# Performance work log

Hardware: AMD Instinct MI355X
Metric: run time of the kernel (lower is better)

## Reference

```python
import jax, jax.numpy as jnp
import numpy as np

RADIUS = 0.1
NSAMPLE = 32
NORMALIZE_XYZ = False
USE_XYZ = True


def ball_query(xyz, center_xyz, radius, nsample):
    """xyz: (B,N,3), center_xyz: (B,S,3) -> idx (B,S,nsample) int32.
    For each center, first `nsample` point indices within `radius`;
    slots with no valid point are filled with the first valid index (0 if none)."""
    N = xyz.shape[1]
    # squared distances (B,S,N)
    d2 = jnp.sum((center_xyz[:, :, None, :] - xyz[:, None, :, :]) ** 2, axis=-1)
    in_ball = d2 < radius * radius
    cand = jnp.where(in_ball, jnp.arange(N, dtype=jnp.int32)[None, None, :], jnp.int32(N))
    cand = jnp.sort(cand, axis=-1)[..., :nsample]  # first nsample in-ball indices
    first = cand[..., :1]
    first = jnp.where(first == N, 0, first)  # fallback to 0 if ball is empty
    idx = jnp.where(cand == N, first, cand)
    return idx


def group(features, idx):
    """features: (B,C,N), idx: (B,S,K) -> (B,C,S,K)"""
    return jax.vmap(lambda f, i: f[:, i])(features, idx)


def setup_inputs() -> dict:
    key = jax.random.key(0)
    k1, k2, k3 = jax.random.split(key, 3)
    B, N, S, C = 4, 8192, 2048, 64
    xyz = jax.random.uniform(k1, (B, N, 3), dtype=jnp.float32)
    center_xyz = jax.random.uniform(k2, (B, S, 3), dtype=jnp.float32)
    features = jax.random.normal(k3, (B, C, N), dtype=jnp.float32)
    return {"xyz": xyz, "center_xyz": center_xyz, "features": features}


def reference(xyz, center_xyz, features):
    idx = ball_query(xyz, center_xyz, RADIUS, NSAMPLE)  # (B,S,K)
    xyz_t = jnp.transpose(xyz, (0, 2, 1))  # (B,3,N)
    grouped_xyz = group(xyz_t, idx)  # (B,3,S,K)
    grouped_xyz = grouped_xyz - jnp.transpose(center_xyz, (0, 2, 1))[..., None]
    if NORMALIZE_XYZ:
        grouped_xyz = grouped_xyz / RADIUS
    grouped_features = group(features, idx)  # (B,C,S,K)
    if USE_XYZ:
        return jnp.concatenate([grouped_xyz, grouped_features], axis=1)  # (B,3+C,S,K)
    return grouped_features
```

## Files before the change

kernel.cpp:

```cpp
#include <hip/hip_runtime.h>
#include <stdint.h>

constexpr int N_PTS = 8192;
constexpr int S_CTR = 2048;
constexpr int BATCH = 4;
constexpr int CHANS = 64;
constexpr int KS = 32;
constexpr int CH_OUT = CHANS + 3;
constexpr int GD = 10;
constexpr int NCELL = GD * GD * GD;
constexpr int CAP = 128;

__device__ __forceinline__ int cell_of(float p) {
    int c = (int)((double)p * 10.0);
    return c < 0 ? 0 : (c > GD - 1 ? GD - 1 : c);
}

__global__ __launch_bounds__(1024) void grid_build(
    const float* __restrict__ xyz, int* __restrict__ cellStart,
    int* __restrict__ sIdx, float* __restrict__ sX,
    float* __restrict__ sY, float* __restrict__ sZ)
{
    __shared__ int cnts[NCELL];
    __shared__ int sc[1024];
    __shared__ int off[NCELL];
    const int b = blockIdx.x, t = threadIdx.x;
    const float* xb = xyz + (size_t)b * N_PTS * 3;

    for (int i = t; i < NCELL; i += 1024) cnts[i] = 0;
    __syncthreads();

    int cellr[8];
#pragma unroll
    for (int j = 0; j < 8; ++j) {
        const int i = t + j * 1024;
        const float x = xb[i * 3], y = xb[i * 3 + 1], z = xb[i * 3 + 2];
        const int c = (cell_of(z) * GD + cell_of(y)) * GD + cell_of(x);
        cellr[j] = c;
        atomicAdd(&cnts[c], 1);
    }
    __syncthreads();

    sc[t] = (t < NCELL) ? cnts[t] : 0;
    __syncthreads();
    for (int o = 1; o < 1024; o <<= 1) {
        const int v = (t >= o) ? sc[t - o] : 0;
        __syncthreads();
        sc[t] += v;
        __syncthreads();
    }
    const int excl = (t == 0) ? 0 : sc[t - 1];
    if (t < NCELL) { cellStart[b * (NCELL + 1) + t] = excl; off[t] = excl; }
    if (t == 0) cellStart[b * (NCELL + 1) + NCELL] = N_PTS;
    __syncthreads();

#pragma unroll
    for (int j = 0; j < 8; ++j) {
        const int i = t + j * 1024;
        const int pos = atomicAdd(&off[cellr[j]], 1);
        sIdx[b * N_PTS + pos] = i;
        sX[b * N_PTS + pos] = xb[i * 3];
        sY[b * N_PTS + pos] = xb[i * 3 + 1];
        sZ[b * N_PTS + pos] = xb[i * 3 + 2];
    }
}

__global__ __launch_bounds__(256) void bq_query(
    const float* __restrict__ ctr, const int* __restrict__ cellStart,
    const int* __restrict__ sIdx, const float* __restrict__ sX,
    const float* __restrict__ sY, const float* __restrict__ sZ,
    int* __restrict__ idx_out)
{
    __shared__ int cand[4][CAP];
    const int wave = threadIdx.x >> 6, lane = threadIdx.x & 63;
    const int cg = blockIdx.x * 4 + wave;
    const int b = cg >> 11;
    const float cx = ctr[(size_t)cg * 3];
    const float cy = ctr[(size_t)cg * 3 + 1];
    const float cz = ctr[(size_t)cg * 3 + 2];
    const float r2 = (float)(0.1 * 0.1);

    const int ix = cell_of(cx), iy = cell_of(cy), iz = cell_of(cz);
    const int xlo = max(ix - 1, 0), xhi = min(ix + 1, GD - 1);
    const int ylo = max(iy - 1, 0), yhi = min(iy + 1, GD - 1);
    const int zlo = max(iz - 1, 0), zhi = min(iz + 1, GD - 1);

    unsigned cnt = 0;
    const int csb = b * (NCELL + 1);
    const int pb = b * N_PTS;

    for (int zz = zlo; zz <= zhi; ++zz)
        for (int yy = ylo; yy <= yhi; ++yy) {
            const int rowc = (zz * GD + yy) * GD;
            const int rs = cellStart[csb + rowc + xlo];
            const int re = cellStart[csb + rowc + xhi + 1];
            for (int p0 = rs; p0 < re; p0 += 64) {
                const int i = p0 + lane;
                const bool valid = i < re;
                float px = 1e9f, py = 1e9f, pz = 1e9f; int oid = 0;
                if (valid) {
                    px = sX[pb + i]; py = sY[pb + i]; pz = sZ[pb + i];
                    oid = sIdx[pb + i];
                }
                const float dx = __fsub_rn(cx, px);
                const float dy = __fsub_rn(cy, py);
                const float dz = __fsub_rn(cz, pz);
                const float d2 = __fadd_rn(
                    __fadd_rn(__fmul_rn(dx, dx), __fmul_rn(dy, dy)),
                    __fmul_rn(dz, dz));
                const bool inb = valid && (d2 < r2);
                const unsigned long long mask = __ballot(inb);
                if (mask) {
                    const unsigned rank = __builtin_amdgcn_mbcnt_hi(
                        (unsigned)(mask >> 32),
                        __builtin_amdgcn_mbcnt_lo((unsigned)mask, 0u));
                    if (inb) {
                        const unsigned slot = cnt + rank;
                        if (slot < (unsigned)CAP) cand[wave][slot] = oid;
                    }
                    cnt += (unsigned)__popcll(mask);
                }
            }
        }
    if (cnt > (unsigned)CAP) cnt = CAP;

    int v0 = (lane < (int)cnt) ? cand[wave][lane] : 0x7fffffff;
    int v1 = (lane + 64 < (int)cnt) ? cand[wave][lane + 64] : 0x7fffffff;
#pragma unroll
    for (int k = 2; k <= 128; k <<= 1) {
        if (k == 128) {
            const int a = min(v0, v1); v1 = max(v0, v1); v0 = a;
        }
#pragma unroll
        for (int j = (k == 128 ? 32 : (k >> 1)); j >= 1; j >>= 1) {
            const int o0 = __shfl_xor(v0, j);
            const int o1 = __shfl_xor(v1, j);
            const bool lower = (lane & j) == 0;
            bool up0, up1;
            if (k == 64)       { up0 = true;  up1 = false; }
            else if (k == 128) { up0 = true;  up1 = true;  }
            else { const bool u = (lane & k) == 0; up0 = u; up1 = u; }
            v0 = (up0 == lower) ? min(v0, o0) : max(v0, o0);
            v1 = (up1 == lower) ? min(v1, o1) : max(v1, o1);
        }
    }

    int first = __shfl(v0, 0);
    if (cnt == 0u) first = 0;
    if (lane < KS) {
        const int val = (lane < (int)cnt) ? v0 : first;
        idx_out[(size_t)cg * KS + lane] = val;
    }
}

__global__ __launch_bounds__(256) void transpose_kernel(
    const float* __restrict__ feat, float* __restrict__ featT)
{
    __shared__ float tile[64][65];
    const int t = threadIdx.x;
    const int n0 = blockIdx.x * 64;
    const int b = blockIdx.y;
    const float* fb = feat + (size_t)b * CHANS * N_PTS;
#pragma unroll
    for (int r = 0; r < 16; ++r) {
        const int c = r * 4 + (t >> 6);
        tile[c][t & 63] = fb[(size_t)c * N_PTS + n0 + (t & 63)];
    }
    __syncthreads();
    float* ob = featT + ((size_t)b * N_PTS + n0) * CHANS;
#pragma unroll
    for (int r = 0; r < 16; ++r) {
        const int n = r * 4 + (t >> 6);
        ob[(size_t)n * CHANS + (t & 63)] = tile[t & 63][n];
    }
}

__global__ __launch_bounds__(256) void gather_kernel(
    const float* __restrict__ xyz, const float* __restrict__ ctr,
    const float* __restrict__ featT, const int* __restrict__ idx_ws,
    float* __restrict__ out)
{
    const int tg = blockIdx.x * 256 + threadIdx.x;
    const int cg = tg >> 5;
    const int k = tg & 31;
    const int b = cg >> 11;
    const int s = cg & (S_CTR - 1);
    const int id = idx_ws[(size_t)cg * KS + k];

    const float* pp = xyz + ((size_t)b * N_PTS + id) * 3;
    const float* cc = ctr + (size_t)cg * 3;
    const float g0 = __fsub_rn(pp[0], cc[0]);
    const float g1 = __fsub_rn(pp[1], cc[1]);
    const float g2 = __fsub_rn(pp[2], cc[2]);

    float f[CHANS];
    const float4* fr = (const float4*)(featT + ((size_t)b * N_PTS + id) * CHANS);
#pragma unroll
    for (int j = 0; j < CHANS / 4; ++j) {
        const float4 v = fr[j];
        f[j * 4 + 0] = v.x; f[j * 4 + 1] = v.y;
        f[j * 4 + 2] = v.z; f[j * 4 + 3] = v.w;
    }

    float* ob = out + ((size_t)b * CH_OUT * S_CTR + s) * KS + k;
    const size_t chs = (size_t)S_CTR * KS;
    ob[0] = g0;
    ob[chs] = g1;
    ob[2 * chs] = g2;
#pragma unroll
    for (int ch = 0; ch < CHANS; ++ch)
        ob[(size_t)(ch + 3) * chs] = f[ch];
}

__global__ __launch_bounds__(256) void bq_brute(
    const float* __restrict__ xyz, const float* __restrict__ ctr,
    int* __restrict__ idx_out)
{
    const int wave = threadIdx.x >> 6, lane = threadIdx.x & 63;
    const int cg = blockIdx.x * 4 + wave;
    const int b = cg >> 11;
    const float* xb = xyz + (size_t)b * N_PTS * 3;
    const float cx = ctr[(size_t)cg * 3], cy = ctr[(size_t)cg * 3 + 1],
                cz = ctr[(size_t)cg * 3 + 2];
    __shared__ int lidx[4][KS];
    unsigned cnt = 0;
    const float r2 = (float)(0.1 * 0.1);
    for (int n0 = 0; n0 < N_PTS && cnt < (unsigned)KS; n0 += 64) {
        const int n = n0 + lane;
        const float px = xb[n * 3], py = xb[n * 3 + 1], pz = xb[n * 3 + 2];
        const float dx = __fsub_rn(cx, px), dy = __fsub_rn(cy, py),
                    dz = __fsub_rn(cz, pz);
        const float d2 = __fadd_rn(
            __fadd_rn(__fmul_rn(dx, dx), __fmul_rn(dy, dy)), __fmul_rn(dz, dz));
        const bool inb = d2 < r2;
        const unsigned long long mask = __ballot(inb);
        if (mask) {
            const unsigned rank = __builtin_amdgcn_mbcnt_hi(
                (unsigned)(mask >> 32),
                __builtin_amdgcn_mbcnt_lo((unsigned)mask, 0u));
            const unsigned slot = cnt + rank;
            if (inb && slot < (unsigned)KS) lidx[wave][slot] = n;
            cnt += (unsigned)__popcll(mask);
        }
    }
    if (cnt > (unsigned)KS) cnt = KS;
    const int first = (cnt > 0) ? lidx[wave][0] : 0;
    if (lane < KS)
        idx_out[(size_t)cg * KS + lane] = (lane < (int)cnt) ? lidx[wave][lane] : first;
}

__global__ __launch_bounds__(256) void gather_direct(
    const float* __restrict__ xyz, const float* __restrict__ ctr,
    const float* __restrict__ feat, const int* __restrict__ idx_ws,
    float* __restrict__ out)
{
    const int wave = threadIdx.x >> 6, lane = threadIdx.x & 63;
    const int cg = blockIdx.x * 4 + wave;
    const int b = cg >> 11;
    const int s = cg & (S_CTR - 1);
    const int k = lane & 31;
    const int half = lane >> 5;
    const int id = idx_ws[(size_t)cg * KS + k];
    const float* pp = xyz + ((size_t)b * N_PTS + id) * 3;
    const float* cc = ctr + (size_t)cg * 3;
    const float g0 = __fsub_rn(pp[0], cc[0]);
    const float g1 = __fsub_rn(pp[1], cc[1]);
    const float g2 = __fsub_rn(pp[2], cc[2]);
    const float* fb = feat + (size_t)b * CHANS * N_PTS + id;
    float* ob = out + ((size_t)b * CH_OUT * S_CTR + s) * KS + k;
    const size_t chs = (size_t)S_CTR * KS;
#pragma unroll
    for (int ch0 = 0; ch0 < CH_OUT; ch0 += 2) {
        const int ch = ch0 + half;
        if (ch < CH_OUT) {
            float v;
            if (ch0 == 0)      v = half ? g1 : g0;
            else if (ch0 == 2) v = half ? fb[0] : g2;
            else               v = fb[(size_t)(ch - 3) * N_PTS];
            ob[(size_t)ch * chs] = v;
        }
    }
}

extern "C" void kernel_launch(void* const* d_in, const int* in_sizes, int n_in,
                              void* d_out, int out_size, void* d_ws, size_t ws_size,
                              hipStream_t stream)
{
    const float* xyz  = (const float*)d_in[0];
    const float* ctr  = (const float*)d_in[1];
    const float* feat = (const float*)d_in[2];
    float* out = (float*)d_out;

    char* w = (char*)d_ws;
    const size_t idx_off   = 0;
    const size_t cs_off    = 1048576;
    const size_t sidx_off  = 1064704;
    const size_t sx_off    = 1195776;
    const size_t sy_off    = 1326848;
    const size_t sz_off    = 1457920;
    const size_t featT_off = 1588992;
    const size_t total_need = featT_off + (size_t)BATCH * N_PTS * CHANS * 4;

    int* idx_ws = (int*)(w + idx_off);

    if (ws_size >= total_need) {
        int*   cellStart = (int*)(w + cs_off);
        int*   sIdx = (int*)(w + sidx_off);
        float* sX = (float*)(w + sx_off);
        float* sY = (float*)(w + sy_off);
        float* sZ = (float*)(w + sz_off);
        float* featT = (float*)(w + featT_off);

        grid_build<<<dim3(BATCH), dim3(1024), 0, stream>>>(
            xyz, cellStart, sIdx, sX, sY, sZ);
        bq_query<<<dim3(BATCH * S_CTR / 4), dim3(256), 0, stream>>>(
            ctr, cellStart, sIdx, sX, sY, sZ, idx_ws);
        transpose_kernel<<<dim3(N_PTS / 64, BATCH), dim3(256), 0, stream>>>(
            feat, featT);
        gather_kernel<<<dim3(BATCH * S_CTR * KS / 256), dim3(256), 0, stream>>>(
            xyz, ctr, featT, idx_ws, out);
    } else {
        bq_brute<<<dim3(BATCH * S_CTR / 4), dim3(256), 0, stream>>>(
            xyz, ctr, idx_ws);
        gather_direct<<<dim3(BATCH * S_CTR / 4), dim3(256), 0, stream>>>(
            xyz, ctr, feat, idx_ws, out);
    }
}
```

Measured before the change: 134.7 us.

## Split grid build into parallel kernels, vectorize transpose and gather with nontemporal stores

Replaces the single-block-per-batch grid build with separate zero, histogram, scan and scatter kernels that use global atomics across many blocks. The feature transpose now uses float4 loads and stores. The gather handles two samples per thread and writes float2 pairs with nontemporal stores to reduce store instructions and cache pollution. This adds kernel launches, and scatter order within a cell now depends on global atomic ordering.

```diff
diff --git a/kernel.cpp b/kernel.cpp
--- a/kernel.cpp
+++ b/kernel.cpp
@@ -16,32 +16,36 @@
     return c < 0 ? 0 : (c > GD - 1 ? GD - 1 : c);
 }
 
-__global__ __launch_bounds__(1024) void grid_build(
-    const float* __restrict__ xyz, int* __restrict__ cellStart,
-    int* __restrict__ sIdx, float* __restrict__ sX,
-    float* __restrict__ sY, float* __restrict__ sZ)
-{
-    __shared__ int cnts[NCELL];
+__device__ __forceinline__ void st_nt2(float2 v, float* p) {
+    double d;
+    __builtin_memcpy(&d, &v, 8);
+    __builtin_nontemporal_store(d, (double*)p);
+}
+
+__global__ __launch_bounds__(256) void zero_cnt(int* __restrict__ p)
+{
+    const int i = blockIdx.x * 256 + threadIdx.x;
+    if (i < BATCH * NCELL) p[i] = 0;
+}
+
+__global__ __launch_bounds__(256) void grid_hist(
+    const float* __restrict__ xyz, int* __restrict__ cellCnt)
+{
+    const int i = blockIdx.x * 256 + threadIdx.x;
+    const int b = i >> 13;
+    const int p = i & (N_PTS - 1);
+    const float* xp = xyz + (size_t)b * N_PTS * 3 + (size_t)p * 3;
+    const int c = (cell_of(xp[2]) * GD + cell_of(xp[1])) * GD + cell_of(xp[0]);
+    atomicAdd(&cellCnt[b * NCELL + c], 1);
+}
+
+__global__ __launch_bounds__(1024) void grid_scan(
+    const int* __restrict__ cellCnt, int* __restrict__ cellStart,
+    int* __restrict__ gOff)
+{
     __shared__ int sc[1024];
-    __shared__ int off[NCELL];
     const int b = blockIdx.x, t = threadIdx.x;
-    const float* xb = xyz + (size_t)b * N_PTS * 3;
-
-    for (int i = t; i < NCELL; i += 1024) cnts[i] = 0;
-    __syncthreads();
-
-    int cellr[8];
-#pragma unroll
-    for (int j = 0; j < 8; ++j) {
-        const int i = t + j * 1024;
-        const float x = xb[i * 3], y = xb[i * 3 + 1], z = xb[i * 3 + 2];
-        const int c = (cell_of(z) * GD + cell_of(y)) * GD + cell_of(x);
-        cellr[j] = c;
-        atomicAdd(&cnts[c], 1);
-    }
-    __syncthreads();
-
-    sc[t] = (t < NCELL) ? cnts[t] : 0;
+    sc[t] = (t < NCELL) ? cellCnt[b * NCELL + t] : 0;
     __syncthreads();
     for (int o = 1; o < 1024; o <<= 1) {
         const int v = (t >= o) ? sc[t - o] : 0;
@@ -50,19 +54,29 @@
         __syncthreads();
     }
     const int excl = (t == 0) ? 0 : sc[t - 1];
-    if (t < NCELL) { cellStart[b * (NCELL + 1) + t] = excl; off[t] = excl; }
+    if (t < NCELL) {
+        cellStart[b * (NCELL + 1) + t] = excl;
+        gOff[b * NCELL + t] = excl;
+    }
     if (t == 0) cellStart[b * (NCELL + 1) + NCELL] = N_PTS;
-    __syncthreads();
-
-#pragma unroll
-    for (int j = 0; j < 8; ++j) {
-        const int i = t + j * 1024;
-        const int pos = atomicAdd(&off[cellr[j]], 1);
-        sIdx[b * N_PTS + pos] = i;
-        sX[b * N_PTS + pos] = xb[i * 3];
-        sY[b * N_PTS + pos] = xb[i * 3 + 1];
-        sZ[b * N_PTS + pos] = xb[i * 3 + 2];
-    }
+}
+
+__global__ __launch_bounds__(256) void grid_scatter(
+    const float* __restrict__ xyz, int* __restrict__ gOff,
+    int* __restrict__ sIdx, float* __restrict__ sX,
+    float* __restrict__ sY, float* __restrict__ sZ)
+{
+    const int i = blockIdx.x * 256 + threadIdx.x;
+    const int b = i >> 13;
+    const int p = i & (N_PTS - 1);
+    const float* xp = xyz + (size_t)b * N_PTS * 3 + (size_t)p * 3;
+    const float x = xp[0], y = xp[1], z = xp[2];
+    const int c = (cell_of(z) * GD + cell_of(y)) * GD + cell_of(x);
+    const int pos = atomicAdd(&gOff[b * NCELL + c], 1);
+    sIdx[b * N_PTS + pos] = p;
+    sX[b * N_PTS + pos] = x;
+    sY[b * N_PTS + pos] = y;
+    sZ[b * N_PTS + pos] = z;
 }
 
 __global__ __launch_bounds__(256) void bq_query(
@@ -162,16 +176,24 @@
     const int b = blockIdx.y;
     const float* fb = feat + (size_t)b * CHANS * N_PTS;
 #pragma unroll
-    for (int r = 0; r < 16; ++r) {
-        const int c = r * 4 + (t >> 6);
-        tile[c][t & 63] = fb[(size_t)c * N_PTS + n0 + (t & 63)];
+    for (int r = 0; r < 4; ++r) {
+        const int c = (t >> 4) + 16 * r;
+        const float4 v =
+            *(const float4*)(fb + (size_t)c * N_PTS + n0 + (t & 15) * 4);
+        tile[c][(t & 15) * 4 + 0] = v.x;
+        tile[c][(t & 15) * 4 + 1] = v.y;
+        tile[c][(t & 15) * 4 + 2] = v.z;
+        tile[c][(t & 15) * 4 + 3] = v.w;
     }
     __syncthreads();
     float* ob = featT + ((size_t)b * N_PTS + n0) * CHANS;
 #pragma unroll
-    for (int r = 0; r < 16; ++r) {
-        const int n = r * 4 + (t >> 6);
-        ob[(size_t)n * CHANS + (t & 63)] = tile[t & 63][n];
+    for (int r = 0; r < 4; ++r) {
+        const int n = (t >> 4) + 16 * r;
+        const int c = (t & 15) * 4;
+        const float4 v = make_float4(tile[c][n], tile[c + 1][n],
+                                     tile[c + 2][n], tile[c + 3][n]);
+        *(float4*)(ob + (size_t)n * CHANS + c) = v;
     }
 }
 
@@ -181,35 +203,37 @@
     float* __restrict__ out)
 {
     const int tg = blockIdx.x * 256 + threadIdx.x;
-    const int cg = tg >> 5;
-    const int k = tg & 31;
+    const int cg = tg >> 4;
+    const int kq = (tg & 15) * 2;
     const int b = cg >> 11;
     const int s = cg & (S_CTR - 1);
-    const int id = idx_ws[(size_t)cg * KS + k];
-
-    const float* pp = xyz + ((size_t)b * N_PTS + id) * 3;
+
+    const int2 id2 = *(const int2*)(idx_ws + (size_t)cg * KS + kq);
     const float* cc = ctr + (size_t)cg * 3;
-    const float g0 = __fsub_rn(pp[0], cc[0]);
-    const float g1 = __fsub_rn(pp[1], cc[1]);
-    const float g2 = __fsub_rn(pp[2], cc[2]);
-
-    float f[CHANS];
-    const float4* fr = (const float4*)(featT + ((size_t)b * N_PTS + id) * CHANS);
-#pragma unroll
-    for (int j = 0; j < CHANS / 4; ++j) {
-        const float4 v = fr[j];
-        f[j * 4 + 0] = v.x; f[j * 4 + 1] = v.y;
-        f[j * 4 + 2] = v.z; f[j * 4 + 3] = v.w;
-    }
-
-    float* ob = out + ((size_t)b * CH_OUT * S_CTR + s) * KS + k;
+    const float cx = cc[0], cy = cc[1], cz = cc[2];
+    const float* pA = xyz + ((size_t)b * N_PTS + id2.x) * 3;
+    const float* pB = xyz + ((size_t)b * N_PTS + id2.y) * 3;
+    const float2 g0 = make_float2(__fsub_rn(pA[0], cx), __fsub_rn(pB[0], cx));
+    const float2 g1 = make_float2(__fsub_rn(pA[1], cy), __fsub_rn(pB[1], cy));
+    const float2 g2 = make_float2(__fsub_rn(pA[2], cz), __fsub_rn(pB[2], cz));
+
+    float* ob = out + ((size_t)b * CH_OUT * S_CTR + s) * KS + kq;
     const size_t chs = (size_t)S_CTR * KS;
-    ob[0] = g0;
-    ob[chs] = g1;
-    ob[2 * chs] = g2;
-#pragma unroll
-    for (int ch = 0; ch < CHANS; ++ch)
-        ob[(size_t)(ch + 3) * chs] = f[ch];
+    st_nt2(g0, ob);
+    st_nt2(g1, ob + chs);
+    st_nt2(g2, ob + 2 * chs);
+
+    const float4* fA = (const float4*)(featT + ((size_t)b * N_PTS + id2.x) * CHANS);
+    const float4* fB = (const float4*)(featT + ((size_t)b * N_PTS + id2.y) * CHANS);
+#pragma unroll
+    for (int t4 = 0; t4 < 16; ++t4) {
+        const float4 a = fA[t4];
+        const float4 c4 = fB[t4];
+        st_nt2(make_float2(a.x, c4.x), ob + (size_t)(3 + t4 * 4 + 0) * chs);
+        st_nt2(make_float2(a.y, c4.y), ob + (size_t)(3 + t4 * 4 + 1) * chs);
+        st_nt2(make_float2(a.z, c4.z), ob + (size_t)(3 + t4 * 4 + 2) * chs);
+        st_nt2(make_float2(a.w, c4.w), ob + (size_t)(3 + t4 * 4 + 3) * chs);
+    }
 }
 
 __global__ __launch_bounds__(256) void bq_brute(
@@ -292,32 +316,42 @@
     float* out = (float*)d_out;
 
     char* w = (char*)d_ws;
-    const size_t idx_off   = 0;
-    const size_t cs_off    = 1048576;
-    const size_t sidx_off  = 1064704;
-    const size_t sx_off    = 1195776;
-    const size_t sy_off    = 1326848;
-    const size_t sz_off    = 1457920;
-    const size_t featT_off = 1588992;
+    const size_t idx_off    = 0;
+    const size_t cnt_off    = 1048576;
+    const size_t cs_off     = cnt_off + 16384;
+    const size_t goff_off   = cs_off + 16384;
+    const size_t sidx_off   = goff_off + 16384;
+    const size_t sx_off     = sidx_off + 131072;
+    const size_t sy_off     = sx_off + 131072;
+    const size_t sz_off     = sy_off + 131072;
+    const size_t featT_off  = sz_off + 131072;
     const size_t total_need = featT_off + (size_t)BATCH * N_PTS * CHANS * 4;
 
     int* idx_ws = (int*)(w + idx_off);
 
     if (ws_size >= total_need) {
+        int*   cellCnt   = (int*)(w + cnt_off);
         int*   cellStart = (int*)(w + cs_off);
-        int*   sIdx = (int*)(w + sidx_off);
-        float* sX = (float*)(w + sx_off);
-        float* sY = (float*)(w + sy_off);
-        float* sZ = (float*)(w + sz_off);
-        float* featT = (float*)(w + featT_off);
-
-        grid_build<<<dim3(BATCH), dim3(1024), 0, stream>>>(
-            xyz, cellStart, sIdx, sX, sY, sZ);
+        int*   gOff      = (int*)(w + goff_off);
+        int*   sIdx      = (int*)(w + sidx_off);
+        float* sX        = (float*)(w + sx_off);
+        float* sY        = (float*)(w + sy_off);
+        float* sZ        = (float*)(w + sz_off);
+        float* featT     = (float*)(w + featT_off);
+
+        zero_cnt<<<dim3((BATCH * NCELL + 255) / 256), dim3(256), 0, stream>>>(
+            cellCnt);
+        grid_hist<<<dim3(BATCH * N_PTS / 256), dim3(256), 0, stream>>>(
+            xyz, cellCnt);
+        grid_scan<<<dim3(BATCH), dim3(1024), 0, stream>>>(
+            cellCnt, cellStart, gOff);
+        grid_scatter<<<dim3(BATCH * N_PTS / 256), dim3(256), 0, stream>>>(
+            xyz, gOff, sIdx, sX, sY, sZ);
         bq_query<<<dim3(BATCH * S_CTR / 4), dim3(256), 0, stream>>>(
             ctr, cellStart, sIdx, sX, sY, sZ, idx_ws);
         transpose_kernel<<<dim3(N_PTS / 64, BATCH), dim3(256), 0, stream>>>(
             feat, featT);
-        gather_kernel<<<dim3(BATCH * S_CTR * KS / 256), dim3(256), 0, stream>>>(
+        gather_kernel<<<dim3(BATCH * S_CTR * KS / 2 / 256), dim3(256), 0, stream>>>(
             xyz, ctr, featT, idx_ws, out);
     } else {
         bq_brute<<<dim3(BATCH * S_CTR / 4), dim3(256), 0, stream>>>(
```

After: 123.7 us. -8.2%, faster.

## Fuse ball query with gather and merge histogram with feature transpose

Applied to the files above, without the earlier changes.

The ball-query kernel now writes the grouped output directly, each wave's two 32-lane halves splitting the 67 output channels, so the idx workspace round trip and the separate gather launch are gone. The grid build is split into a histogram/scan step that runs in the same launch as a float4-vectorised feature transpose, followed by a fully parallel scatter kernel in place of a single 1024-thread block per batch. Sorted points are packed as float4 (x,y,z,index) so one vector load replaces four. Output stores are nontemporal. In exchange, each wave now issues all 67 channel writes after its query, and the scatter's global atomics make the order of points within a cell nondeterministic, which the later sort has to absorb.

```diff
diff --git a/kernel.cpp b/kernel.cpp
--- a/kernel.cpp
+++ b/kernel.cpp
@@ -16,65 +16,99 @@
     return c < 0 ? 0 : (c > GD - 1 ? GD - 1 : c);
 }
 
-__global__ __launch_bounds__(1024) void grid_build(
-    const float* __restrict__ xyz, int* __restrict__ cellStart,
-    int* __restrict__ sIdx, float* __restrict__ sX,
-    float* __restrict__ sY, float* __restrict__ sZ)
-{
-    __shared__ int cnts[NCELL];
-    __shared__ int sc[1024];
-    __shared__ int off[NCELL];
-    const int b = blockIdx.x, t = threadIdx.x;
-    const float* xb = xyz + (size_t)b * N_PTS * 3;
-
-    for (int i = t; i < NCELL; i += 1024) cnts[i] = 0;
-    __syncthreads();
-
-    int cellr[8];
-#pragma unroll
-    for (int j = 0; j < 8; ++j) {
-        const int i = t + j * 1024;
-        const float x = xb[i * 3], y = xb[i * 3 + 1], z = xb[i * 3 + 2];
-        const int c = (cell_of(z) * GD + cell_of(y)) * GD + cell_of(x);
-        cellr[j] = c;
-        atomicAdd(&cnts[c], 1);
-    }
-    __syncthreads();
-
-    sc[t] = (t < NCELL) ? cnts[t] : 0;
-    __syncthreads();
-    for (int o = 1; o < 1024; o <<= 1) {
-        const int v = (t >= o) ? sc[t - o] : 0;
+#define Q_EL(l) (((l) & 3) == 0 ? q[(l) >> 2].x : ((l) & 3) == 1 ? q[(l) >> 2].y \
+               : ((l) & 3) == 2 ? q[(l) >> 2].z : q[(l) >> 2].w)
+
+__global__ __launch_bounds__(256) void histscan_transpose(
+    const float* __restrict__ xyz, const float* __restrict__ feat,
+    int* __restrict__ cellStart, int* __restrict__ gOff,
+    float* __restrict__ featT)
+{
+    if (blockIdx.x < (unsigned)BATCH) {
+        __shared__ int cnts[1024];
+        __shared__ int part[256];
+        const int b = blockIdx.x, t = threadIdx.x;
+        cnts[t] = 0; cnts[t + 256] = 0; cnts[t + 512] = 0; cnts[t + 768] = 0;
         __syncthreads();
-        sc[t] += v;
+        const float* xb = xyz + (size_t)b * N_PTS * 3;
+        for (int j = 0; j < 32; ++j) {
+            const int i = t + j * 256;
+            const float x = xb[i * 3], y = xb[i * 3 + 1], z = xb[i * 3 + 2];
+            atomicAdd(&cnts[(cell_of(z) * GD + cell_of(y)) * GD + cell_of(x)], 1);
+        }
         __syncthreads();
-    }
-    const int excl = (t == 0) ? 0 : sc[t - 1];
-    if (t < NCELL) { cellStart[b * (NCELL + 1) + t] = excl; off[t] = excl; }
-    if (t == 0) cellStart[b * (NCELL + 1) + NCELL] = N_PTS;
-    __syncthreads();
-
-#pragma unroll
-    for (int j = 0; j < 8; ++j) {
-        const int i = t + j * 1024;
-        const int pos = atomicAdd(&off[cellr[j]], 1);
-        sIdx[b * N_PTS + pos] = i;
-        sX[b * N_PTS + pos] = xb[i * 3];
-        sY[b * N_PTS + pos] = xb[i * 3 + 1];
-        sZ[b * N_PTS + pos] = xb[i * 3 + 2];
-    }
-}
-
-__global__ __launch_bounds__(256) void bq_query(
-    const float* __restrict__ ctr, const int* __restrict__ cellStart,
-    const int* __restrict__ sIdx, const float* __restrict__ sX,
-    const float* __restrict__ sY, const float* __restrict__ sZ,
-    int* __restrict__ idx_out)
+        const int c0 = cnts[4 * t], c1 = cnts[4 * t + 1],
+                  c2 = cnts[4 * t + 2], c3 = cnts[4 * t + 3];
+        part[t] = c0 + c1 + c2 + c3;
+        __syncthreads();
+        for (int o = 1; o < 256; o <<= 1) {
+            const int v = (t >= o) ? part[t - o] : 0;
+            __syncthreads();
+            part[t] += v;
+            __syncthreads();
+        }
+        const int base = (t == 0) ? 0 : part[t - 1];
+        const int e0 = base, e1 = base + c0, e2 = e1 + c1, e3 = e2 + c2;
+        const int cb = b * (NCELL + 1);
+        if (4 * t + 0 < NCELL) { cellStart[cb + 4 * t + 0] = e0; gOff[b * NCELL + 4 * t + 0] = e0; }
+        if (4 * t + 1 < NCELL) { cellStart[cb + 4 * t + 1] = e1; gOff[b * NCELL + 4 * t + 1] = e1; }
+        if (4 * t + 2 < NCELL) { cellStart[cb + 4 * t + 2] = e2; gOff[b * NCELL + 4 * t + 2] = e2; }
+        if (4 * t + 3 < NCELL) { cellStart[cb + 4 * t + 3] = e3; gOff[b * NCELL + 4 * t + 3] = e3; }
+        if (t == 0) cellStart[cb + NCELL] = N_PTS;
+    } else {
+        __shared__ float tile[64][65];
+        const int bx = blockIdx.x - BATCH;
+        const int t = threadIdx.x;
+        const int n0 = (bx & 127) * 64;
+        const int b = bx >> 7;
+        const float* fb = feat + (size_t)b * CHANS * N_PTS;
+#pragma unroll
+        for (int r = 0; r < 4; ++r) {
+            const int c = (t >> 4) + 16 * r;
+            const float4 v =
+                *(const float4*)(fb + (size_t)c * N_PTS + n0 + (t & 15) * 4);
+            tile[c][(t & 15) * 4 + 0] = v.x;
+            tile[c][(t & 15) * 4 + 1] = v.y;
+            tile[c][(t & 15) * 4 + 2] = v.z;
+            tile[c][(t & 15) * 4 + 3] = v.w;
+        }
+        __syncthreads();
+        float* ob = featT + ((size_t)b * N_PTS + n0) * CHANS;
+#pragma unroll
+        for (int r = 0; r < 4; ++r) {
+            const int n = (t >> 4) + 16 * r;
+            const int c = (t & 15) * 4;
+            const float4 v = make_float4(tile[c][n], tile[c + 1][n],
+                                         tile[c + 2][n], tile[c + 3][n]);
+            *(float4*)(ob + (size_t)n * CHANS + c) = v;
+        }
+    }
+}
+
+__global__ __launch_bounds__(256) void grid_scatter(
+    const float* __restrict__ xyz, int* __restrict__ gOff,
+    float4* __restrict__ sPts)
+{
+    const int i = blockIdx.x * 256 + threadIdx.x;
+    const int b = i >> 13;
+    const int p = i & (N_PTS - 1);
+    const float* xp = xyz + (size_t)b * N_PTS * 3 + (size_t)p * 3;
+    const float x = xp[0], y = xp[1], z = xp[2];
+    const int c = (cell_of(z) * GD + cell_of(y)) * GD + cell_of(x);
+    const int pos = atomicAdd(&gOff[b * NCELL + c], 1);
+    sPts[b * N_PTS + pos] = make_float4(x, y, z, __int_as_float(p));
+}
+
+__global__ __launch_bounds__(256) void bq_gather(
+    const float* __restrict__ xyz, const float* __restrict__ ctr,
+    const int* __restrict__ cellStart, const float4* __restrict__ sPts,
+    const float* __restrict__ featT, float* __restrict__ out)
 {
     __shared__ int cand[4][CAP];
     const int wave = threadIdx.x >> 6, lane = threadIdx.x & 63;
     const int cg = blockIdx.x * 4 + wave;
     const int b = cg >> 11;
+    const int s = cg & (S_CTR - 1);
     const float cx = ctr[(size_t)cg * 3];
     const float cy = ctr[(size_t)cg * 3 + 1];
     const float cz = ctr[(size_t)cg * 3 + 2];
@@ -99,8 +133,8 @@
                 const bool valid = i < re;
                 float px = 1e9f, py = 1e9f, pz = 1e9f; int oid = 0;
                 if (valid) {
-                    px = sX[pb + i]; py = sY[pb + i]; pz = sZ[pb + i];
-                    oid = sIdx[pb + i];
+                    const float4 v = sPts[pb + i];
+                    px = v.x; py = v.y; pz = v.z; oid = __float_as_int(v.w);
                 }
                 const float dx = __fsub_rn(cx, px);
                 const float dy = __fsub_rn(cy, py);
@@ -147,69 +181,36 @@
 
     int first = __shfl(v0, 0);
     if (cnt == 0u) first = 0;
-    if (lane < KS) {
-        const int val = (lane < (int)cnt) ? v0 : first;
-        idx_out[(size_t)cg * KS + lane] = val;
-    }
-}
-
-__global__ __launch_bounds__(256) void transpose_kernel(
-    const float* __restrict__ feat, float* __restrict__ featT)
-{
-    __shared__ float tile[64][65];
-    const int t = threadIdx.x;
-    const int n0 = blockIdx.x * 64;
-    const int b = blockIdx.y;
-    const float* fb = feat + (size_t)b * CHANS * N_PTS;
-#pragma unroll
-    for (int r = 0; r < 16; ++r) {
-        const int c = r * 4 + (t >> 6);
-        tile[c][t & 63] = fb[(size_t)c * N_PTS + n0 + (t & 63)];
-    }
-    __syncthreads();
-    float* ob = featT + ((size_t)b * N_PTS + n0) * CHANS;
-#pragma unroll
-    for (int r = 0; r < 16; ++r) {
-        const int n = r * 4 + (t >> 6);
-        ob[(size_t)n * CHANS + (t & 63)] = tile[t & 63][n];
-    }
-}
-
-__global__ __launch_bounds__(256) void gather_kernel(
-    const float* __restrict__ xyz, const float* __restrict__ ctr,
-    const float* __restrict__ featT, const int* __restrict__ idx_ws,
-    float* __restrict__ out)
-{
-    const int tg = blockIdx.x * 256 + threadIdx.x;
-    const int cg = tg >> 5;
-    const int k = tg & 31;
-    const int b = cg >> 11;
-    const int s = cg & (S_CTR - 1);
-    const int id = idx_ws[(size_t)cg * KS + k];
+    const int k = lane & 31;
+    const int v0k = __shfl(v0, k);
+    const int id = (k < (int)cnt) ? v0k : first;
 
     const float* pp = xyz + ((size_t)b * N_PTS + id) * 3;
-    const float* cc = ctr + (size_t)cg * 3;
-    const float g0 = __fsub_rn(pp[0], cc[0]);
-    const float g1 = __fsub_rn(pp[1], cc[1]);
-    const float g2 = __fsub_rn(pp[2], cc[2]);
-
-    float f[CHANS];
-    const float4* fr = (const float4*)(featT + ((size_t)b * N_PTS + id) * CHANS);
-#pragma unroll
-    for (int j = 0; j < CHANS / 4; ++j) {
-        const float4 v = fr[j];
-        f[j * 4 + 0] = v.x; f[j * 4 + 1] = v.y;
-        f[j * 4 + 2] = v.z; f[j * 4 + 3] = v.w;
-    }
-
+    const float g0 = __fsub_rn(pp[0], cx);
+    const float g1 = __fsub_rn(pp[1], cy);
+    const float g2 = __fsub_rn(pp[2], cz);
+
+    const int h = lane >> 5;
+    const size_t chs = (size_t)S_CTR * KS;
     float* ob = out + ((size_t)b * CH_OUT * S_CTR + s) * KS + k;
-    const size_t chs = (size_t)S_CTR * KS;
-    ob[0] = g0;
-    ob[chs] = g1;
-    ob[2 * chs] = g2;
-#pragma unroll
-    for (int ch = 0; ch < CHANS; ++ch)
-        ob[(size_t)(ch + 3) * chs] = f[ch];
+    float* obh = ob + (size_t)(34 * h) * chs;
+
+    const float4* fq =
+        (const float4*)(featT + ((size_t)b * N_PTS + id) * CHANS) + 7 * h;
+    float4 q[9];
+#pragma unroll
+    for (int j = 0; j < 9; ++j) q[j] = fq[j];
+
+    __builtin_nontemporal_store(h ? q[0].w : g0, obh);
+    __builtin_nontemporal_store(h ? q[1].x : g1, obh + chs);
+    __builtin_nontemporal_store(h ? q[1].y : g2, obh + 2 * chs);
+#pragma unroll
+    for (int i = 3; i <= 32; ++i) {
+        const float d = h ? Q_EL(i + 3) : Q_EL(i - 3);
+        __builtin_nontemporal_store(d, obh + (size_t)i * chs);
+    }
+    if (!h)
+        __builtin_nontemporal_store(Q_EL(30), obh + (size_t)33 * chs);
 }
 
 __global__ __launch_bounds__(256) void bq_brute(
@@ -292,34 +293,26 @@
     float* out = (float*)d_out;
 
     char* w = (char*)d_ws;
-    const size_t idx_off   = 0;
-    const size_t cs_off    = 1048576;
-    const size_t sidx_off  = 1064704;
-    const size_t sx_off    = 1195776;
-    const size_t sy_off    = 1326848;
-    const size_t sz_off    = 1457920;
-    const size_t featT_off = 1588992;
+    const size_t cs_off    = 0;
+    const size_t goff_off  = 16384;
+    const size_t spts_off  = 32768;
+    const size_t featT_off = 32768 + 524288;
     const size_t total_need = featT_off + (size_t)BATCH * N_PTS * CHANS * 4;
 
-    int* idx_ws = (int*)(w + idx_off);
-
     if (ws_size >= total_need) {
-        int*   cellStart = (int*)(w + cs_off);
-        int*   sIdx = (int*)(w + sidx_off);
-        float* sX = (float*)(w + sx_off);
-        float* sY = (float*)(w + sy_off);
-        float* sZ = (float*)(w + sz_off);
-        float* featT = (float*)(w + featT_off);
-
-        grid_build<<<dim3(BATCH), dim3(1024), 0, stream>>>(
-            xyz, cellStart, sIdx, sX, sY, sZ);
-        bq_query<<<dim3(BATCH * S_CTR / 4), dim3(256), 0, stream>>>(
-            ctr, cellStart, sIdx, sX, sY, sZ, idx_ws);
-        transpose_kernel<<<dim3(N_PTS / 64, BATCH), dim3(256), 0, stream>>>(
-            feat, featT);
-        gather_kernel<<<dim3(BATCH * S_CTR * KS / 256), dim3(256), 0, stream>>>(
-            xyz, ctr, featT, idx_ws, out);
+        int*    cellStart = (int*)(w + cs_off);
+        int*    gOff      = (int*)(w + goff_off);
+        float4* sPts      = (float4*)(w + spts_off);
+        float*  featT     = (float*)(w + featT_off);
+
+        histscan_transpose<<<dim3(BATCH + BATCH * (N_PTS / 64)), dim3(256),
+                             0, stream>>>(xyz, feat, cellStart, gOff, featT);
+        grid_scatter<<<dim3(BATCH * N_PTS / 256), dim3(256), 0, stream>>>(
+            xyz, gOff, sPts);
+        bq_gather<<<dim3(BATCH * S_CTR / 4), dim3(256), 0, stream>>>(
+            xyz, ctr, cellStart, sPts, featT, out);
     } else {
+        int* idx_ws = (int*)w;
         bq_brute<<<dim3(BATCH * S_CTR / 4), dim3(256), 0, stream>>>(
             xyz, ctr, idx_ws);
         gather_direct<<<dim3(BATCH * S_CTR / 4), dim3(256), 0, stream>>>(
```

New measurement: 118.6 us (median of 2 runs). -12.0%, faster.
